# Kernel optimization log

Hardware: AMD Instinct MI355X
Metric: run time of the kernel (lower is better)

## Reference

```python
import jax, jax.numpy as jnp
import numpy as np

D_IN = 16
D_OUT = 8
HIDDEN = 64


def setup_inputs() -> dict:
    key = jax.random.key(0)
    ks = jax.random.split(key, 8)
    B = 524288
    x = jax.random.normal(ks[0], (B, D_IN), dtype=jnp.float32)
    # scalar attention weights for the two attention blocks, shape [2, 1]
    wq = jax.random.normal(ks[1], (2, 1), dtype=jnp.float32)
    wk = jax.random.normal(ks[2], (2, 1), dtype=jnp.float32)
    wv = jax.random.normal(ks[3], (2, 1), dtype=jnp.float32)
    # hidden: Linear(16 -> HIDDEN), output: Linear(HIDDEN -> 8)
    lim_h = 1.0 / np.sqrt(D_IN)
    Wh = jax.random.uniform(ks[4], (HIDDEN, D_IN), minval=-lim_h, maxval=lim_h, dtype=jnp.float32)
    bh = jax.random.uniform(ks[5], (HIDDEN,), minval=-lim_h, maxval=lim_h, dtype=jnp.float32)
    lim_o = 1.0 / np.sqrt(HIDDEN)
    Wo = jax.random.uniform(ks[6], (D_OUT, HIDDEN), minval=-lim_o, maxval=lim_o, dtype=jnp.float32)
    bo = jax.random.uniform(ks[7], (D_OUT,), minval=-lim_o, maxval=lim_o, dtype=jnp.float32)
    return {"x": x, "wq": wq, "wk": wk, "wv": wv, "Wh": Wh, "bh": bh, "Wo": Wo, "bo": bo}


def _self_attention(x, q, k, v):
    # x: [B, D]; q, k, v: scalars. Q=K=V are scalar-scaled copies of x.
    Q = q * x  # [B, D]
    K = k * x
    V = v * x
    # Alpha[b, i, j] = K[b, i] * Q[b, j]  (outer product, matches Kt @ Q)
    Alpha = K[:, :, None] * Q[:, None, :]  # [B, D, D]
    A = jax.nn.softmax(Alpha, axis=2)
    # O[b, j] = sum_i V[b, i] * A[b, i, j]  (matches V @ AlphaD)
    return jnp.einsum('bi,bij->bj', V, A)  # [B, D]


def reference(x, wq, wk, wv, Wh, bh, Wo, bo):
    o1 = _self_attention(x[:, 0:16], wq[0, 0], wk[0, 0], wv[0, 0])  # [B, 16]
    x1 = jax.nn.sigmoid(o1 @ Wh.T + bh)                              # [B, HIDDEN]
    x2 = x1 @ Wo.T + bo                                              # [B, 8]
    o2 = _self_attention(x2, wq[1, 0], wk[1, 0], wv[1, 0])          # [B, 8]
    w = jax.nn.softmax(o2, axis=1)                                   # [B, 8]
    # out = x[:, None, 8:16] @ w[:, :, None]  -> [B, 1, 1]
    out = jnp.einsum('bi,bi->b', x[:, 8:16], w)[:, None, None]
    return out
```

## Files before the change

### kernel.cpp

```cpp
#include <hip/hip_runtime.h>


typedef float v2f __attribute__((ext_vector_type(2)));

#define LOG2E 1.44269504088896340736f
#define ROWS 2

__device__ __forceinline__ float rcpf(float a) { return __builtin_amdgcn_rcpf(a); }

#if __has_builtin(__builtin_amdgcn_exp2f)
__device__ __forceinline__ float exp2_fast(float a) { return __builtin_amdgcn_exp2f(a); }
#else
__device__ __forceinline__ float exp2_fast(float a) { return __expf(0.6931471805599453f * a); }
#endif

__global__ __launch_bounds__(256, 4) void fused_attn_mlp(
    const float* __restrict__ x,
    const float* __restrict__ wq,
    const float* __restrict__ wk,
    const float* __restrict__ wv,
    const float* __restrict__ Wh,
    const float* __restrict__ bh,
    const float* __restrict__ Wo,
    const float* __restrict__ bo,
    float* __restrict__ out,
    int B)
{
    __shared__ float sWh[64 * 16];
    __shared__ float sWoT[64 * 8];
    __shared__ float sbh[64];

    const int t = threadIdx.x;
    {
        const float4* src = reinterpret_cast<const float4*>(Wh);
        float4* dst = reinterpret_cast<float4*>(sWh);
        dst[t] = src[t];
    }
    #pragma unroll
    for (int r = t; r < 512; r += 256) {
        const int h = r >> 3, o = r & 7;
        sWoT[h * 8 + o] = Wo[o * 64 + h];
    }
    if (t < 64) sbh[t] = bh[t];
    __syncthreads();

    const int b0 = blockIdx.x * (256 * ROWS) + t;
    bool valid[ROWS];
    #pragma unroll
    for (int r = 0; r < ROWS; ++r) valid[r] = (b0 + r * 256) < B;

    float xs[ROWS][16];
    v2f xv2[ROWS][8];
    #pragma unroll
    for (int r = 0; r < ROWS; ++r) {
        if (valid[r]) {
            const float4* xr = reinterpret_cast<const float4*>(x) + (size_t)(b0 + r * 256) * 4;
            float4 a0 = xr[0], a1 = xr[1], a2 = xr[2], a3 = xr[3];
            xs[r][0]=a0.x; xs[r][1]=a0.y; xs[r][2]=a0.z; xs[r][3]=a0.w;
            xs[r][4]=a1.x; xs[r][5]=a1.y; xs[r][6]=a1.z; xs[r][7]=a1.w;
            xs[r][8]=a2.x; xs[r][9]=a2.y; xs[r][10]=a2.z; xs[r][11]=a2.w;
            xs[r][12]=a3.x; xs[r][13]=a3.y; xs[r][14]=a3.z; xs[r][15]=a3.w;
        } else {
            #pragma unroll
            for (int i = 0; i < 16; ++i) xs[r][i] = 0.f;
        }
        #pragma unroll
        for (int p = 0; p < 8; ++p) { v2f v; v[0]=xs[r][2*p]; v[1]=xs[r][2*p+1]; xv2[r][p]=v; }
    }

    const float kq1 = wk[0] * wq[0] * LOG2E;
    const float v1  = wv[0];

    float xmx[ROWS], xmn[ROWS];
    #pragma unroll
    for (int r = 0; r < ROWS; ++r) {
        float mx = xs[r][0], mn = xs[r][0];
        #pragma unroll
        for (int i = 1; i < 16; ++i) { mx = fmaxf(mx, xs[r][i]); mn = fminf(mn, xs[r][i]); }
        xmx[r] = mx; xmn[r] = mn;
    }

    v2f o1v[ROWS][8];
    #pragma unroll
    for (int r = 0; r < ROWS; ++r)
        #pragma unroll
        for (int p = 0; p < 8; ++p) o1v[r][p] = (v2f)(0.f);

    #pragma unroll
    for (int i = 0; i < 16; ++i) {
        v2f e2[ROWS][8];
        float w[ROWS];
        #pragma unroll
        for (int r = 0; r < ROWS; ++r) {
            const float c = kq1 * xs[r][i];
            const float m = fmaxf(c * xmx[r], c * xmn[r]);
            v2f cc; cc[0]=c; cc[1]=c;
            v2f mm; mm[0]=m; mm[1]=m;
            v2f sv = (v2f)(0.f);
            #pragma unroll
            for (int p = 0; p < 8; ++p) {
                v2f a = cc * xv2[r][p] - mm;
                v2f e; e[0] = exp2_fast(a[0]); e[1] = exp2_fast(a[1]);
                e2[r][p] = e;
                sv += e;
            }
            w[r] = v1 * xs[r][i] * rcpf(sv[0] + sv[1]);
        }
        #pragma unroll
        for (int r = 0; r < ROWS; ++r) {
            v2f ww; ww[0]=w[r]; ww[1]=w[r];
            #pragma unroll
            for (int p = 0; p < 8; ++p) o1v[r][p] += ww * e2[r][p];
        }
    }

    v2f x2v[ROWS][4];
    #pragma unroll
    for (int r = 0; r < ROWS; ++r)
        #pragma unroll
        for (int p = 0; p < 4; ++p) { v2f v; v[0]=bo[2*p]; v[1]=bo[2*p+1]; x2v[r][p]=v; }

    #pragma unroll 4
    for (int h = 0; h < 64; ++h) {
        const v2f* wh = reinterpret_cast<const v2f*>(sWh + h * 16);
        v2f whr[8];
        #pragma unroll
        for (int p = 0; p < 8; ++p) whr[p] = wh[p];
        float sg[ROWS];
        #pragma unroll
        for (int r = 0; r < ROWS; ++r) {
            v2f acc = whr[0] * o1v[r][0];
            #pragma unroll
            for (int p = 1; p < 8; ++p) acc += whr[p] * o1v[r][p];
            const float a = acc[0] + acc[1] + sbh[h];
            sg[r] = rcpf(1.f + exp2_fast(-a * LOG2E));
        }
        const v2f* wo = reinterpret_cast<const v2f*>(sWoT + h * 8);
        v2f wor[4];
        #pragma unroll
        for (int p = 0; p < 4; ++p) wor[p] = wo[p];
        #pragma unroll
        for (int r = 0; r < ROWS; ++r) {
            v2f sgv; sgv[0]=sg[r]; sgv[1]=sg[r];
            #pragma unroll
            for (int p = 0; p < 4; ++p) x2v[r][p] += wor[p] * sgv;
        }
    }

    const float kq2 = wk[1] * wq[1] * LOG2E;
    const float v2s = wv[1] * LOG2E;

    float ys[ROWS][8];
    float ymx[ROWS], ymn[ROWS];
    #pragma unroll
    for (int r = 0; r < ROWS; ++r) {
        #pragma unroll
        for (int i = 0; i < 8; ++i) ys[r][i] = x2v[r][i >> 1][i & 1];
        float mx = ys[r][0], mn = ys[r][0];
        #pragma unroll
        for (int i = 1; i < 8; ++i) { mx = fmaxf(mx, ys[r][i]); mn = fminf(mn, ys[r][i]); }
        ymx[r] = mx; ymn[r] = mn;
    }

    v2f o2v[ROWS][4];
    #pragma unroll
    for (int r = 0; r < ROWS; ++r)
        #pragma unroll
        for (int p = 0; p < 4; ++p) o2v[r][p] = (v2f)(0.f);

    #pragma unroll
    for (int i = 0; i < 8; ++i) {
        v2f e2[ROWS][4];
        float w[ROWS];
        #pragma unroll
        for (int r = 0; r < ROWS; ++r) {
            const float c = kq2 * ys[r][i];
            const float m = fmaxf(c * ymx[r], c * ymn[r]);
            v2f cc; cc[0]=c; cc[1]=c;
            v2f mm; mm[0]=m; mm[1]=m;
            v2f sv = (v2f)(0.f);
            #pragma unroll
            for (int p = 0; p < 4; ++p) {
                v2f a = cc * x2v[r][p] - mm;
                v2f e; e[0] = exp2_fast(a[0]); e[1] = exp2_fast(a[1]);
                e2[r][p] = e;
                sv += e;
            }
            w[r] = v2s * ys[r][i] * rcpf(sv[0] + sv[1]);
        }
        #pragma unroll
        for (int r = 0; r < ROWS; ++r) {
            v2f ww; ww[0]=w[r]; ww[1]=w[r];
            #pragma unroll
            for (int p = 0; p < 4; ++p) o2v[r][p] += ww * e2[r][p];
        }
    }

    #pragma unroll
    for (int r = 0; r < ROWS; ++r) {
        float o2s[8];
        #pragma unroll
        for (int i = 0; i < 8; ++i) o2s[i] = o2v[r][i >> 1][i & 1];
        float m2 = o2s[0];
        #pragma unroll
        for (int i = 1; i < 8; ++i) m2 = fmaxf(m2, o2s[i]);
        float s2 = 0.f, dot = 0.f;
        #pragma unroll
        for (int i = 0; i < 8; ++i) {
            const float e = exp2_fast(o2s[i] - m2);
            s2 += e;
            dot += xs[r][8 + i] * e;
        }
        if (valid[r]) out[b0 + r * 256] = dot * rcpf(s2);
    }
}

extern "C" void kernel_launch(void* const* d_in, const int* in_sizes, int n_in,
                              void* d_out, int out_size, void* d_ws, size_t ws_size,
                              hipStream_t stream) {
    const float* x  = (const float*)d_in[0];
    const float* wq = (const float*)d_in[1];
    const float* wk = (const float*)d_in[2];
    const float* wv = (const float*)d_in[3];
    const float* Wh = (const float*)d_in[4];
    const float* bh = (const float*)d_in[5];
    const float* Wo = (const float*)d_in[6];
    const float* bo = (const float*)d_in[7];
    float* out = (float*)d_out;

    const int B = in_sizes[0] / 16;
    const int block = 256;
    const int rows_per_block = block * ROWS;
    const int grid = (B + rows_per_block - 1) / rows_per_block;
    fused_attn_mlp<<<grid, block, 0, stream>>>(x, wq, wk, wv, Wh, bh, Wo, bo, out, B);
}
```

Before: 127.3 us.

## Replace hardware exp2 with packed polynomial exp2 and batch sigmoid reciprocals

Swaps the transcendental-unit exp2 for a degree-5 polynomial evaluated on packed float2 FMAs, using rint and ldexp for the exponent. The hidden-layer sigmoid is regrouped into blocks of four, so one reciprocal plus a product-tree trick replaces four reciprocals. The final softmax is also vectorized. The aim is to move work off the quarter-rate transcendental unit onto packed FMA throughput. The cost is many more ALU instructions per exp, plus the rint/ldexp conversions, which are not packed. The polynomial also has slightly lower accuracy.

```diff
diff --git a/kernel.cpp b/kernel.cpp
--- a/kernel.cpp
+++ b/kernel.cpp
@@ -8,11 +8,22 @@
 
 __device__ __forceinline__ float rcpf(float a) { return __builtin_amdgcn_rcpf(a); }
 
-#if __has_builtin(__builtin_amdgcn_exp2f)
-__device__ __forceinline__ float exp2_fast(float a) { return __builtin_amdgcn_exp2f(a); }
-#else
-__device__ __forceinline__ float exp2_fast(float a) { return __expf(0.6931471805599453f * a); }
-#endif
+__device__ __forceinline__ v2f pexp2(v2f a) {
+    a = __builtin_elementwise_max(a, (v2f)(-126.f));
+    v2f kf;
+    kf[0] = __builtin_rintf(a[0]);
+    kf[1] = __builtin_rintf(a[1]);
+    v2f f = a - kf;
+    v2f p = (v2f)(0.0096181291076285f);
+    p = p * f + (v2f)(0.0555041086648216f);
+    p = p * f + (v2f)(0.2402265069591007f);
+    p = p * f + (v2f)(0.6931471805599453f);
+    p = p * f + (v2f)(1.0f);
+    v2f r;
+    r[0] = ldexpf(p[0], (int)kf[0]);
+    r[1] = ldexpf(p[1], (int)kf[1]);
+    return r;
+}
 
 __global__ __launch_bounds__(256, 4) void fused_attn_mlp(
     const float* __restrict__ x,
@@ -99,8 +110,7 @@
             v2f sv = (v2f)(0.f);
             #pragma unroll
             for (int p = 0; p < 8; ++p) {
-                v2f a = cc * xv2[r][p] - mm;
-                v2f e; e[0] = exp2_fast(a[0]); e[1] = exp2_fast(a[1]);
+                v2f e = pexp2(cc * xv2[r][p] - mm);
                 e2[r][p] = e;
                 sv += e;
             }
@@ -120,30 +130,58 @@
         #pragma unroll
         for (int p = 0; p < 4; ++p) { v2f v; v[0]=bo[2*p]; v[1]=bo[2*p+1]; x2v[r][p]=v; }
 
-    #pragma unroll 4
-    for (int h = 0; h < 64; ++h) {
-        const v2f* wh = reinterpret_cast<const v2f*>(sWh + h * 16);
-        v2f whr[8];
-        #pragma unroll
-        for (int p = 0; p < 8; ++p) whr[p] = wh[p];
-        float sg[ROWS];
-        #pragma unroll
-        for (int r = 0; r < ROWS; ++r) {
-            v2f acc = whr[0] * o1v[r][0];
-            #pragma unroll
-            for (int p = 1; p < 8; ++p) acc += whr[p] * o1v[r][p];
-            const float a = acc[0] + acc[1] + sbh[h];
-            sg[r] = rcpf(1.f + exp2_fast(-a * LOG2E));
-        }
-        const v2f* wo = reinterpret_cast<const v2f*>(sWoT + h * 8);
-        v2f wor[4];
-        #pragma unroll
-        for (int p = 0; p < 4; ++p) wor[p] = wo[p];
-        #pragma unroll
-        for (int r = 0; r < ROWS; ++r) {
-            v2f sgv; sgv[0]=sg[r]; sgv[1]=sg[r];
-            #pragma unroll
-            for (int p = 0; p < 4; ++p) x2v[r][p] += wor[p] * sgv;
+    #pragma unroll 2
+    for (int g = 0; g < 16; ++g) {
+        float apre[ROWS][4];
+        #pragma unroll
+        for (int hh = 0; hh < 4; ++hh) {
+            const int h = g * 4 + hh;
+            const v2f* wh = reinterpret_cast<const v2f*>(sWh + h * 16);
+            v2f whr[8];
+            #pragma unroll
+            for (int p = 0; p < 8; ++p) whr[p] = wh[p];
+            #pragma unroll
+            for (int r = 0; r < ROWS; ++r) {
+                v2f acc = whr[0] * o1v[r][0];
+                #pragma unroll
+                for (int p = 1; p < 8; ++p) acc += whr[p] * o1v[r][p];
+                apre[r][hh] = acc[0] + acc[1] + sbh[h];
+            }
+        }
+        float sg[ROWS][4];
+        #pragma unroll
+        for (int r = 0; r < ROWS; ++r) {
+            v2f la0; la0[0] = apre[r][0]; la0[1] = apre[r][1];
+            v2f la1; la1[0] = apre[r][2]; la1[1] = apre[r][3];
+            la0 = __builtin_elementwise_min(la0 * (v2f)(-LOG2E), (v2f)(30.f));
+            la1 = __builtin_elementwise_min(la1 * (v2f)(-LOG2E), (v2f)(30.f));
+            v2f e0 = pexp2(la0), e1 = pexp2(la1);
+            const float d0 = 1.f + e0[0], d1 = 1.f + e0[1];
+            const float d2 = 1.f + e1[0], d3 = 1.f + e1[1];
+            const float p01  = d0 * d1;
+            const float p012 = p01 * d2;
+            const float rq   = rcpf(p012 * d3);
+            const float i3 = rq * p012;
+            const float tq = rq * d3;
+            const float i2 = tq * p01;
+            const float t2 = tq * d2;
+            const float i1 = t2 * d0;
+            const float i0 = t2 * d1;
+            sg[r][0]=i0; sg[r][1]=i1; sg[r][2]=i2; sg[r][3]=i3;
+        }
+        #pragma unroll
+        for (int hh = 0; hh < 4; ++hh) {
+            const int h = g * 4 + hh;
+            const v2f* wo = reinterpret_cast<const v2f*>(sWoT + h * 8);
+            v2f wor[4];
+            #pragma unroll
+            for (int p = 0; p < 4; ++p) wor[p] = wo[p];
+            #pragma unroll
+            for (int r = 0; r < ROWS; ++r) {
+                v2f sgv; sgv[0]=sg[r][hh]; sgv[1]=sg[r][hh];
+                #pragma unroll
+                for (int p = 0; p < 4; ++p) x2v[r][p] += wor[p] * sgv;
+            }
         }
     }
 
@@ -181,8 +219,7 @@
             v2f sv = (v2f)(0.f);
             #pragma unroll
             for (int p = 0; p < 4; ++p) {
-                v2f a = cc * x2v[r][p] - mm;
-                v2f e; e[0] = exp2_fast(a[0]); e[1] = exp2_fast(a[1]);
+                v2f e = pexp2(cc * x2v[r][p] - mm);
                 e2[r][p] = e;
                 sv += e;
             }
@@ -204,14 +241,16 @@
         float m2 = o2s[0];
         #pragma unroll
         for (int i = 1; i < 8; ++i) m2 = fmaxf(m2, o2s[i]);
-        float s2 = 0.f, dot = 0.f;
-        #pragma unroll
-        for (int i = 0; i < 8; ++i) {
-            const float e = exp2_fast(o2s[i] - m2);
-            s2 += e;
-            dot += xs[r][8 + i] * e;
-        }
-        if (valid[r]) out[b0 + r * 256] = dot * rcpf(s2);
+        v2f mm2; mm2[0]=m2; mm2[1]=m2;
+        v2f se = (v2f)(0.f), de = (v2f)(0.f);
+        #pragma unroll
+        for (int p = 0; p < 4; ++p) {
+            v2f e = pexp2(o2v[r][p] - mm2);
+            se += e;
+            v2f xp; xp[0]=xs[r][8+2*p]; xp[1]=xs[r][9+2*p];
+            de += xp * e;
+        }
+        if (valid[r]) out[b0 + r * 256] = (de[0] + de[1]) * rcpf(se[0] + se[1]);
     }
 }
 
```

After: 149.2 us. +17.2%, slower.

## Batch sigmoid reciprocals across four hidden units and tree-reduce softmax sums

Applied to the files above, without the earlier changes.

The hidden-layer loop now handles groups of four units. For each group it computes four denominators and replaces four rcp calls with one rcp plus a product-tree trick (Montgomery batch inversion). The exponent input is clamped at 30 to prevent overflow in the product. The softmax sums become pairwise tree reductions, which shortens dependency chains, and the final softmax-dot is vectorized with packed v2f ops. This cuts transcendental (rcp) instructions and adds extra multiplies. It also risks precision loss when denominators are large.

```diff
diff --git a/kernel.cpp b/kernel.cpp
--- a/kernel.cpp
+++ b/kernel.cpp
@@ -96,14 +96,19 @@
             const float m = fmaxf(c * xmx[r], c * xmn[r]);
             v2f cc; cc[0]=c; cc[1]=c;
             v2f mm; mm[0]=m; mm[1]=m;
-            v2f sv = (v2f)(0.f);
             #pragma unroll
             for (int p = 0; p < 8; ++p) {
                 v2f a = cc * xv2[r][p] - mm;
                 v2f e; e[0] = exp2_fast(a[0]); e[1] = exp2_fast(a[1]);
                 e2[r][p] = e;
-                sv += e;
-            }
+            }
+            v2f s01 = e2[r][0] + e2[r][1];
+            v2f s23 = e2[r][2] + e2[r][3];
+            v2f s45 = e2[r][4] + e2[r][5];
+            v2f s67 = e2[r][6] + e2[r][7];
+            v2f s03 = s01 + s23;
+            v2f s47 = s45 + s67;
+            v2f sv  = s03 + s47;
             w[r] = v1 * xs[r][i] * rcpf(sv[0] + sv[1]);
         }
         #pragma unroll
@@ -120,30 +125,58 @@
         #pragma unroll
         for (int p = 0; p < 4; ++p) { v2f v; v[0]=bo[2*p]; v[1]=bo[2*p+1]; x2v[r][p]=v; }
 
-    #pragma unroll 4
-    for (int h = 0; h < 64; ++h) {
-        const v2f* wh = reinterpret_cast<const v2f*>(sWh + h * 16);
-        v2f whr[8];
-        #pragma unroll
-        for (int p = 0; p < 8; ++p) whr[p] = wh[p];
-        float sg[ROWS];
-        #pragma unroll
-        for (int r = 0; r < ROWS; ++r) {
-            v2f acc = whr[0] * o1v[r][0];
-            #pragma unroll
-            for (int p = 1; p < 8; ++p) acc += whr[p] * o1v[r][p];
-            const float a = acc[0] + acc[1] + sbh[h];
-            sg[r] = rcpf(1.f + exp2_fast(-a * LOG2E));
-        }
-        const v2f* wo = reinterpret_cast<const v2f*>(sWoT + h * 8);
-        v2f wor[4];
-        #pragma unroll
-        for (int p = 0; p < 4; ++p) wor[p] = wo[p];
-        #pragma unroll
-        for (int r = 0; r < ROWS; ++r) {
-            v2f sgv; sgv[0]=sg[r]; sgv[1]=sg[r];
-            #pragma unroll
-            for (int p = 0; p < 4; ++p) x2v[r][p] += wor[p] * sgv;
+    #pragma unroll 2
+    for (int g = 0; g < 16; ++g) {
+        float apre[ROWS][4];
+        #pragma unroll
+        for (int hh = 0; hh < 4; ++hh) {
+            const int h = g * 4 + hh;
+            const v2f* wh = reinterpret_cast<const v2f*>(sWh + h * 16);
+            v2f whr[8];
+            #pragma unroll
+            for (int p = 0; p < 8; ++p) whr[p] = wh[p];
+            #pragma unroll
+            for (int r = 0; r < ROWS; ++r) {
+                v2f acc = whr[0] * o1v[r][0];
+                #pragma unroll
+                for (int p = 1; p < 8; ++p) acc += whr[p] * o1v[r][p];
+                apre[r][hh] = acc[0] + acc[1] + sbh[h];
+            }
+        }
+        float sg[ROWS][4];
+        #pragma unroll
+        for (int r = 0; r < ROWS; ++r) {
+            float d[4];
+            #pragma unroll
+            for (int hh = 0; hh < 4; ++hh) {
+                const float la = fminf(-apre[r][hh] * LOG2E, 30.f);
+                d[hh] = 1.f + exp2_fast(la);
+            }
+            const float p01  = d[0] * d[1];
+            const float p012 = p01 * d[2];
+            const float rq   = rcpf(p012 * d[3]);
+            const float i3 = rq * p012;
+            const float tq = rq * d[3];
+            const float i2 = tq * p01;
+            const float t2 = tq * d[2];
+            sg[r][0] = t2 * d[1];
+            sg[r][1] = t2 * d[0];
+            sg[r][2] = i2;
+            sg[r][3] = i3;
+        }
+        #pragma unroll
+        for (int hh = 0; hh < 4; ++hh) {
+            const int h = g * 4 + hh;
+            const v2f* wo = reinterpret_cast<const v2f*>(sWoT + h * 8);
+            v2f wor[4];
+            #pragma unroll
+            for (int p = 0; p < 4; ++p) wor[p] = wo[p];
+            #pragma unroll
+            for (int r = 0; r < ROWS; ++r) {
+                v2f sgv; sgv[0]=sg[r][hh]; sgv[1]=sg[r][hh];
+                #pragma unroll
+                for (int p = 0; p < 4; ++p) x2v[r][p] += wor[p] * sgv;
+            }
         }
     }
 
@@ -178,14 +211,15 @@
             const float m = fmaxf(c * ymx[r], c * ymn[r]);
             v2f cc; cc[0]=c; cc[1]=c;
             v2f mm; mm[0]=m; mm[1]=m;
-            v2f sv = (v2f)(0.f);
             #pragma unroll
             for (int p = 0; p < 4; ++p) {
                 v2f a = cc * x2v[r][p] - mm;
                 v2f e; e[0] = exp2_fast(a[0]); e[1] = exp2_fast(a[1]);
                 e2[r][p] = e;
-                sv += e;
-            }
+            }
+            v2f s01 = e2[r][0] + e2[r][1];
+            v2f s23 = e2[r][2] + e2[r][3];
+            v2f sv  = s01 + s23;
             w[r] = v2s * ys[r][i] * rcpf(sv[0] + sv[1]);
         }
         #pragma unroll
@@ -204,14 +238,17 @@
         float m2 = o2s[0];
         #pragma unroll
         for (int i = 1; i < 8; ++i) m2 = fmaxf(m2, o2s[i]);
-        float s2 = 0.f, dot = 0.f;
-        #pragma unroll
-        for (int i = 0; i < 8; ++i) {
-            const float e = exp2_fast(o2s[i] - m2);
-            s2 += e;
-            dot += xs[r][8 + i] * e;
-        }
-        if (valid[r]) out[b0 + r * 256] = dot * rcpf(s2);
+        v2f mm2; mm2[0]=m2; mm2[1]=m2;
+        v2f se = (v2f)(0.f), de = (v2f)(0.f);
+        #pragma unroll
+        for (int p = 0; p < 4; ++p) {
+            v2f a = o2v[r][p] - mm2;
+            v2f e; e[0] = exp2_fast(a[0]); e[1] = exp2_fast(a[1]);
+            se += e;
+            v2f xp; xp[0]=xs[r][8+2*p]; xp[1]=xs[r][9+2*p];
+            de += xp * e;
+        }
+        if (valid[r]) out[b0 + r * 256] = (de[0] + de[1]) * rcpf(se[0] + se[1]);
     }
 }
 
```

Result: slower. 133.2 us (+4.6%).
